# Kernel tuning notes

Hardware: AMD Instinct MI355X
Metric: run time of the kernel (lower is better)

Reference implementation:

```python
import jax, jax.numpy as jnp
import numpy as np

# Acoustic FDTD constants (seistorch-style geometry)
NSHOTS, NT = 4, 512
NZ, NX = 256, 256
NRECS = 128
DT = 1e-3   # s
DH = 10.0   # m grid spacing


def setup_inputs() -> dict:
    key = jax.random.key(0)
    k1, k2, k3, k4, k5, k6 = jax.random.split(key, 6)
    x = jax.random.normal(k1, (NSHOTS, NT), dtype=jnp.float32)  # source wavelets
    # velocity model in [1500, 4000] m/s (CFL: dt*vmax/dh = 0.4 < stability limit)
    vp = 1500.0 + 2500.0 * jax.random.uniform(k2, (NZ, NX), dtype=jnp.float32)
    src_z = jax.random.randint(k3, (NSHOTS,), 0, NZ)
    src_x = jax.random.randint(k4, (NSHOTS,), 0, NX)
    rec_z = jax.random.randint(k5, (NSHOTS, NRECS), 0, NZ)
    rec_x = jax.random.randint(k6, (NSHOTS, NRECS), 0, NX)
    return {"x": x, "vp": vp, "src_z": src_z, "src_x": src_x,
            "rec_z": rec_z, "rec_x": rec_x}


def _laplacian(p):
    # 5-point stencil, zero Dirichlet boundary. p: (B, NZ, NX)
    pp = jnp.pad(p, ((0, 0), (1, 1), (1, 1)))
    return (pp[:, 2:, 1:-1] + pp[:, :-2, 1:-1]
            + pp[:, 1:-1, 2:] + pp[:, 1:-1, :-2]
            - 4.0 * p) / (DH * DH)


def reference(x, vp, src_z, src_x, rec_z, rec_x):
    shots = jnp.arange(NSHOTS)
    c2dt2 = (vp * DT) ** 2  # (NZ, NX), broadcast over shots

    def step(carry, wav_t):
        p_prev, p = carry
        # 2nd-order acoustic update (the PDE "cell")
        p_next = 2.0 * p - p_prev + c2dt2 * _laplacian(p)
        # source scatter-inject (super_source)
        p_next = p_next.at[shots, src_z, src_x].add(wav_t * DT * DT)
        # receiver gather (super_probes): (NSHOTS, NRECS)
        rec = p_next[shots[:, None], rec_z, rec_x]
        return (p, p_next), rec

    p0 = jnp.zeros((NSHOTS, NZ, NX), dtype=x.dtype)
    _, recs = jax.lax.scan(step, (p0, p0), x.T)  # recs: (NT, NSHOTS, NRECS)
    # (shots, time, receivers, n_receiver_types=1)
    return jnp.transpose(recs, (1, 0, 2))[..., None]
```

## Files before the change

### kernel.cpp

```cpp
#include <hip/hip_runtime.h>

#define NSHOTS 4
#define NT     512
#define NZ     256
#define NX     256
#define NRECS  128

static constexpr float DTf    = 0.001f;
static constexpr float INVDH2 = 1.0f / (10.0f * 10.0f);

#define KSTEPS 16
#define TILE   32
#define RPT    8
#define NPAIRS 4
#define NWAVES 8
#define BLOCK  512
#define NWG    (NSHOTS * 64)
#define NPHASE (NT / KSTEPS)
#define LSTRIDE 32

typedef float v2f __attribute__((ext_vector_type(2)));

__device__ __forceinline__ float nbr_left(float v) {
  return __int_as_float(__builtin_amdgcn_update_dpp(
      0, __float_as_int(v), 0x138 , 0xf, 0xf, true));
}
__device__ __forceinline__ float nbr_right(float v) {
  return __int_as_float(__builtin_amdgcn_update_dpp(
      0, __float_as_int(v), 0x130 , 0xf, 0xf, true));
}

__device__ __forceinline__ float gload(const float* p) {
  return __hip_atomic_load(p, __ATOMIC_RELAXED, __HIP_MEMORY_SCOPE_AGENT);
}
__device__ __forceinline__ void gstore(float* p, float v) {
  __hip_atomic_store(p, v, __ATOMIC_RELAXED, __HIP_MEMORY_SCOPE_AGENT);
}
__device__ __forceinline__ unsigned fload(const unsigned* p) {
  return __hip_atomic_load(p, __ATOMIC_RELAXED, __HIP_MEMORY_SCOPE_AGENT);
}
__device__ __forceinline__ void fstore(unsigned* p, unsigned v) {
  __hip_atomic_store(p, v, __ATOMIC_RELAXED, __HIP_MEMORY_SCOPE_AGENT);
}

__global__ __launch_bounds__(BLOCK, 4) void wave_pk(
    float* __restrict__ f0c, float* __restrict__ f0p,
    float* __restrict__ f1c, float* __restrict__ f1p,
    const float* __restrict__ vp, const float* __restrict__ xwav,
    const int* __restrict__ src_z, const int* __restrict__ src_x,
    const int* __restrict__ rec_z, const int* __restrict__ rec_x,
    float* __restrict__ out,
    unsigned* __restrict__ bar)
{
  const int bid  = blockIdx.x;
  const int s    = bid >> 6;
  const int tz   = (bid >> 3) & 7;
  const int tx   = bid & 7;
  const int tid  = threadIdx.x;
  const int w    = tid >> 6;
  const int lane = tid & 63;

  const int gz0 = tz * TILE - KSTEPS;
  const int gx0 = tx * TILE - KSTEPS;
  const int gx  = gx0 + lane;
  const int zb  = w * RPT;

  __shared__ float haloTop[2][NWAVES][64];
  __shared__ float haloBot[2][NWAVES][64];
  __shared__ float recTile[2][TILE][TILE + 1];
  __shared__ int   cntS;
  __shared__ int   lzA[NRECS], lxA[NRECS];
  __shared__ unsigned pkA[NRECS];

  if (tid == 0) cntS = 0;
  __syncthreads();
  if (tid < NRECS) {
    const int lz = rec_z[s * NRECS + tid] - tz * TILE;
    const int lx = rec_x[s * NRECS + tid] - tx * TILE;
    lzA[tid] = lz; lxA[tid] = lx;
    if ((unsigned)lz < (unsigned)TILE && (unsigned)lx < (unsigned)TILE) {
      const int k = atomicAdd(&cntS, 1);
      pkA[k] = (unsigned)tid | ((unsigned)lz << 8) | ((unsigned)lx << 16);
    }
  }
  __syncthreads();
  const int nRec = cntS;
  int myR = 0, myLz = 0, myLx = 0;
  if (tid < nRec) {
    const unsigned p = pkA[tid];
    myR = p & 255; myLz = (p >> 8) & 31; myLx = (p >> 16) & 31;
  }
  const bool wbRow = (w >= 2 && w < 6) && (lane >= KSTEPS && lane < KSTEPS + TILE);
  const int  ilz   = (w - 2) * RPT;
  const int  ilx   = lane - KSTEPS;
  unsigned recMask = 0;
  if (wbRow) {
    for (int r = 0; r < NRECS; ++r)
      if (lxA[r] == ilx && (unsigned)(lzA[r] - ilz) < (unsigned)RPT)
        recMask |= 1u << (lzA[r] - ilz);
  }

  int nb = -1;
  if (tid < 8) {
    const int k  = (tid < 4) ? tid : tid + 1;
    const int dz = k / 3 - 1, dx = k % 3 - 1;
    const int qz = tz + dz, qx = tx + dx;
    if ((unsigned)qz < 8u && (unsigned)qx < 8u)
      nb = (s << 6) | (qz << 3) | qx;
  }
  unsigned* wF = bar;
  unsigned* rF = bar + (size_t)NWG * LSTRIDE;

  auto pollGE = [&](unsigned* base, unsigned target) {
    if (nb >= 0) {
      while (fload(base + (size_t)nb * LSTRIDE) < target)
        __builtin_amdgcn_s_sleep(1);
    }
  };

  const int slz = src_z[s] - gz0;
  const int slx = src_x[s] - gx0;
  const bool srcMine = (slx == lane) && ((unsigned)(slz - zb) < (unsigned)RPT);
  const int  srcI = slz - zb;
  v2f srcM2[NPAIRS];
  #pragma unroll
  for (int p = 0; p < NPAIRS; ++p) {
    srcM2[p].x = (srcMine && srcI == 2 * p)     ? 1.0f : 0.0f;
    srcM2[p].y = (srcMine && srcI == 2 * p + 1) ? 1.0f : 0.0f;
  }

  const bool xok = (unsigned)gx < (unsigned)NX;
  int   offRow[RPT];
  bool  okRow[RPT];
  v2f a2[NPAIRS], b2[NPAIRS], c22[NPAIRS], d22[NPAIRS];
  #pragma unroll
  for (int p = 0; p < NPAIRS; ++p) {
    #pragma unroll
    for (int h = 0; h < 2; ++h) {
      const int i  = 2 * p + h;
      const int gz = gz0 + zb + i;
      const bool ok = xok && ((unsigned)gz < (unsigned)NZ);
      okRow[i]  = ok;
      offRow[i] = ok ? ((s * NZ + gz) * NX + gx) : 0;
      float v = ok ? vp[gz * NX + gx] : 0.0f;
      v *= DTf;
      const float c2 = v * v * INVDH2;
      if (h == 0) { c22[p].x = c2; d22[p].x = 2.0f - 4.0f * c2; }
      else        { c22[p].y = c2; d22[p].y = 2.0f - 4.0f * c2; }
    }
    a2[p] = (v2f)(0.0f); b2[p] = (v2f)(0.0f);
  }

  #pragma unroll 1
  for (int ph = 0; ph < NPHASE; ++ph) {
    const int t0 = ph * KSTEPS;

    if (ph > 0) {
      pollGE(wF, (unsigned)ph);
      __syncthreads();
      const float* rc = (ph & 1) ? f0c : f1c;
      const float* rp = (ph & 1) ? f0p : f1p;
      if (!wbRow) {
        #pragma unroll
        for (int p = 0; p < NPAIRS; ++p) {
          a2[p].x = okRow[2 * p]     ? gload(rc + offRow[2 * p])     : 0.0f;
          a2[p].y = okRow[2 * p + 1] ? gload(rc + offRow[2 * p + 1]) : 0.0f;
          b2[p].x = okRow[2 * p]     ? gload(rp + offRow[2 * p])     : 0.0f;
          b2[p].y = okRow[2 * p + 1] ? gload(rp + offRow[2 * p + 1]) : 0.0f;
        }
      }
      __builtin_amdgcn_s_waitcnt(0);
      __syncthreads();
      if (tid == 0) fstore(rF + (size_t)bid * LSTRIDE, (unsigned)ph);
    }

    float amp[KSTEPS];
    {
      const float4* xw4 = (const float4*)(xwav + s * NT + t0);
      #pragma unroll
      for (int q = 0; q < KSTEPS / 4; ++q) {
        const float4 v = xw4[q];
        amp[4 * q + 0] = (v.x * DTf) * DTf;
        amp[4 * q + 1] = (v.y * DTf) * DTf;
        amp[4 * q + 2] = (v.z * DTf) * DTf;
        amp[4 * q + 3] = (v.w * DTf) * DTf;
      }
    }

    float recv[KSTEPS];

    auto do_step = [&](v2f (&cur)[NPAIRS], v2f (&nxt)[NPAIRS], int tau) {
      const int pb = tau & 1;
      haloTop[pb][w][lane] = cur[0].x;
      haloBot[pb][w][lane] = cur[NPAIRS - 1].y;
      __syncthreads();
      if (tau > 0 && tid < nRec) recv[tau - 1] = recTile[1 - pb][myLz][myLx];
      const float up0 = (w > 0)          ? haloBot[pb][w - 1][lane] : 0.0f;
      const float dn7 = (w < NWAVES - 1) ? haloTop[pb][w + 1][lane] : 0.0f;
      const v2f av = { amp[tau], amp[tau] };
      #pragma unroll
      for (int p = 0; p < NPAIRS; ++p) {
        const float cx = cur[p].x, cy = cur[p].y;
        const float upx = (p == 0)          ? up0 : cur[p - 1].y;
        const float dny = (p == NPAIRS - 1) ? dn7 : cur[p + 1].x;
        v2f ud, lr;
        ud.x = upx + cy;
        ud.y = cx + dny;
        lr.x = nbr_left(cx) + nbr_right(cx);
        lr.y = nbr_left(cy) + nbr_right(cy);
        const v2f sum = ud + lr;
        v2f t = __builtin_elementwise_fma(c22[p], sum, -nxt[p]);
        t = __builtin_elementwise_fma(d22[p], cur[p], t);
        t = __builtin_elementwise_fma(srcM2[p], av, t);
        nxt[p] = t;
      }
      if (recMask) {
        #pragma unroll
        for (int i = 0; i < RPT; ++i)
          if (recMask & (1u << i))
            recTile[pb][ilz + i][ilx] = (i & 1) ? nxt[i >> 1].y : nxt[i >> 1].x;
      }
    };

    #pragma unroll
    for (int h = 0; h < KSTEPS / 2; ++h) {
      do_step(a2, b2, 2 * h);
      do_step(b2, a2, 2 * h + 1);
    }

    if (ph >= 2 && ph != NPHASE - 1) pollGE(rF, (unsigned)(ph - 1));
    __syncthreads();
    if (tid < nRec) recv[KSTEPS - 1] = recTile[1][myLz][myLx];

    if (tid < nRec) {
      #pragma unroll
      for (int t = 0; t < KSTEPS; ++t)
        out[(s * NT + (t0 + t)) * NRECS + myR] = recv[t];
    }

    if (ph != NPHASE - 1) {
      float* wc = (ph & 1) ? f1c : f0c;
      float* wp = (ph & 1) ? f1p : f0p;
      if (wbRow) {
        #pragma unroll
        for (int p = 0; p < NPAIRS; ++p) {
          gstore(wc + offRow[2 * p],     a2[p].x);
          gstore(wc + offRow[2 * p + 1], a2[p].y);
          gstore(wp + offRow[2 * p],     b2[p].x);
          gstore(wp + offRow[2 * p + 1], b2[p].y);
        }
      }
      __builtin_amdgcn_s_waitcnt(0);
      __syncthreads();
      if (tid == 0) fstore(wF + (size_t)bid * LSTRIDE, (unsigned)(ph + 1));
    }
  }
}

extern "C" void kernel_launch(void* const* d_in, const int* in_sizes, int n_in,
                              void* d_out, int out_size, void* d_ws, size_t ws_size,
                              hipStream_t stream) {
  const float* x     = (const float*)d_in[0];
  const float* vp    = (const float*)d_in[1];
  const int*   src_z = (const int*)d_in[2];
  const int*   src_x = (const int*)d_in[3];
  const int*   rec_z = (const int*)d_in[4];
  const int*   rec_x = (const int*)d_in[5];
  float* out = (float*)d_out;

  float* ws = (float*)d_ws;
  const size_t F = (size_t)NSHOTS * NZ * NX;
  float* f0c = ws;
  float* f0p = ws + F;
  float* f1c = ws + 2 * F;
  float* f1p = ws + 3 * F;
  unsigned* bar = (unsigned*)(ws + 4 * F);

  hipMemsetAsync(bar, 0, 2 * (size_t)NWG * LSTRIDE * sizeof(unsigned), stream);

  wave_pk<<<dim3(NWG), dim3(BLOCK), 0, stream>>>(
      f0c, f0p, f1c, f1p, vp, x, src_z, src_x, rec_z, rec_x, out, bar);
}
```

Measured before the change: 324.4 us.

## Triple-buffer halo slabs to drop read-flag barrier and specialize source injection

Replaces the double-buffered exchange fields with three rotating slabs. The separate read-done flags, and the polling on them before overwriting a buffer, can then be removed, leaving only one write-flag wait per phase. Neighbor polling moves from the first threads to lane<8 of every wave, so each wave waits on its own and the block-wide sync after polling is gone. The source FMA is compiled out for tiles whose extended region lacks the source, and the receiver output stores move after the flag publish so they no longer delay neighbors. The cost is more workspace memory and reliance on the three-slab rotation being enough to stop a block overwriting data a slow neighbor has not read yet.

Result: slower. 400.9 us (+23.6%).

```diff
diff --git a/kernel.cpp b/kernel.cpp
--- a/kernel.cpp
+++ b/kernel.cpp
@@ -1,4 +1,5 @@
 #include <hip/hip_runtime.h>
+#include <type_traits>
 
 #define NSHOTS 4
 #define NT     512
@@ -11,13 +12,16 @@
 
 #define KSTEPS 16
 #define TILE   32
+#define EXT    64
 #define RPT    8
 #define NPAIRS 4
 #define NWAVES 8
 #define BLOCK  512
 #define NWG    (NSHOTS * 64)
 #define NPHASE (NT / KSTEPS)
+#define NSLAB  3
 #define LSTRIDE 32
+#define FCNT   (NSHOTS * NZ * NX)
 
 typedef float v2f __attribute__((ext_vector_type(2)));
 
@@ -43,14 +47,13 @@
   __hip_atomic_store(p, v, __ATOMIC_RELAXED, __HIP_MEMORY_SCOPE_AGENT);
 }
 
-__global__ __launch_bounds__(BLOCK, 4) void wave_pk(
-    float* __restrict__ f0c, float* __restrict__ f0p,
-    float* __restrict__ f1c, float* __restrict__ f1p,
+__global__ __launch_bounds__(BLOCK, 4) void wave_pk3(
+    float* __restrict__ fld,
     const float* __restrict__ vp, const float* __restrict__ xwav,
     const int* __restrict__ src_z, const int* __restrict__ src_x,
     const int* __restrict__ rec_z, const int* __restrict__ rec_x,
     float* __restrict__ out,
-    unsigned* __restrict__ bar)
+    unsigned* __restrict__ wF)
 {
   const int bid  = blockIdx.x;
   const int s    = bid >> 6;
@@ -101,25 +104,23 @@
   }
 
   int nb = -1;
-  if (tid < 8) {
-    const int k  = (tid < 4) ? tid : tid + 1;
+  if (lane < 8) {
+    const int k  = (lane < 4) ? lane : lane + 1;
     const int dz = k / 3 - 1, dx = k % 3 - 1;
     const int qz = tz + dz, qx = tx + dx;
     if ((unsigned)qz < 8u && (unsigned)qx < 8u)
       nb = (s << 6) | (qz << 3) | qx;
   }
-  unsigned* wF = bar;
-  unsigned* rF = bar + (size_t)NWG * LSTRIDE;
-
-  auto pollGE = [&](unsigned* base, unsigned target) {
+  auto pollGE = [&](unsigned target) {
     if (nb >= 0) {
-      while (fload(base + (size_t)nb * LSTRIDE) < target)
+      while (fload(wF + (size_t)nb * LSTRIDE) < target)
         __builtin_amdgcn_s_sleep(1);
     }
   };
 
   const int slz = src_z[s] - gz0;
   const int slx = src_x[s] - gx0;
+  const bool srcInExt = ((unsigned)slz < (unsigned)EXT) && ((unsigned)slx < (unsigned)EXT);
   const bool srcMine = (slx == lane) && ((unsigned)(slz - zb) < (unsigned)RPT);
   const int  srcI = slz - zb;
   v2f srcM2[NPAIRS];
@@ -151,15 +152,17 @@
     a2[p] = (v2f)(0.0f); b2[p] = (v2f)(0.0f);
   }
 
+  int wsl = 0;
+
   #pragma unroll 1
   for (int ph = 0; ph < NPHASE; ++ph) {
     const int t0 = ph * KSTEPS;
 
     if (ph > 0) {
-      pollGE(wF, (unsigned)ph);
-      __syncthreads();
-      const float* rc = (ph & 1) ? f0c : f1c;
-      const float* rp = (ph & 1) ? f0p : f1p;
+      pollGE((unsigned)ph);
+      const int rsl = (wsl == 0) ? 2 : wsl - 1;
+      const float* rc = fld + (size_t)(2 * rsl) * FCNT;
+      const float* rp = rc + FCNT;
       if (!wbRow) {
         #pragma unroll
         for (int p = 0; p < NPAIRS; ++p) {
@@ -169,9 +172,6 @@
           b2[p].y = okRow[2 * p + 1] ? gload(rp + offRow[2 * p + 1]) : 0.0f;
         }
       }
-      __builtin_amdgcn_s_waitcnt(0);
-      __syncthreads();
-      if (tid == 0) fstore(rF + (size_t)bid * LSTRIDE, (unsigned)ph);
     }
 
     float amp[KSTEPS];
@@ -189,58 +189,55 @@
 
     float recv[KSTEPS];
 
-    auto do_step = [&](v2f (&cur)[NPAIRS], v2f (&nxt)[NPAIRS], int tau) {
-      const int pb = tau & 1;
-      haloTop[pb][w][lane] = cur[0].x;
-      haloBot[pb][w][lane] = cur[NPAIRS - 1].y;
-      __syncthreads();
-      if (tau > 0 && tid < nRec) recv[tau - 1] = recTile[1 - pb][myLz][myLx];
-      const float up0 = (w > 0)          ? haloBot[pb][w - 1][lane] : 0.0f;
-      const float dn7 = (w < NWAVES - 1) ? haloTop[pb][w + 1][lane] : 0.0f;
-      const v2f av = { amp[tau], amp[tau] };
+    auto run_steps = [&](auto srcc) {
+      auto do_step = [&](v2f (&cur)[NPAIRS], v2f (&nxt)[NPAIRS], int tau) {
+        const int pb = tau & 1;
+        haloTop[pb][w][lane] = cur[0].x;
+        haloBot[pb][w][lane] = cur[NPAIRS - 1].y;
+        __syncthreads();
+        if (tau > 0 && tid < nRec) recv[tau - 1] = recTile[1 - pb][myLz][myLx];
+        const float up0 = (w > 0)          ? haloBot[pb][w - 1][lane] : 0.0f;
+        const float dn7 = (w < NWAVES - 1) ? haloTop[pb][w + 1][lane] : 0.0f;
+        const v2f av = { amp[tau], amp[tau] };
+        #pragma unroll
+        for (int p = 0; p < NPAIRS; ++p) {
+          const float cx = cur[p].x, cy = cur[p].y;
+          const float upx = (p == 0)          ? up0 : cur[p - 1].y;
+          const float dny = (p == NPAIRS - 1) ? dn7 : cur[p + 1].x;
+          v2f ud, lr;
+          ud.x = upx + cy;
+          ud.y = cx + dny;
+          lr.x = nbr_left(cx) + nbr_right(cx);
+          lr.y = nbr_left(cy) + nbr_right(cy);
+          const v2f sum = ud + lr;
+          v2f t = __builtin_elementwise_fma(c22[p], sum, -nxt[p]);
+          t = __builtin_elementwise_fma(d22[p], cur[p], t);
+          if constexpr (decltype(srcc)::value)
+            t = __builtin_elementwise_fma(srcM2[p], av, t);
+          nxt[p] = t;
+        }
+        if (recMask) {
+          #pragma unroll
+          for (int i = 0; i < RPT; ++i)
+            if (recMask & (1u << i))
+              recTile[pb][ilz + i][ilx] = (i & 1) ? nxt[i >> 1].y : nxt[i >> 1].x;
+        }
+      };
       #pragma unroll
-      for (int p = 0; p < NPAIRS; ++p) {
-        const float cx = cur[p].x, cy = cur[p].y;
-        const float upx = (p == 0)          ? up0 : cur[p - 1].y;
-        const float dny = (p == NPAIRS - 1) ? dn7 : cur[p + 1].x;
-        v2f ud, lr;
-        ud.x = upx + cy;
-        ud.y = cx + dny;
-        lr.x = nbr_left(cx) + nbr_right(cx);
-        lr.y = nbr_left(cy) + nbr_right(cy);
-        const v2f sum = ud + lr;
-        v2f t = __builtin_elementwise_fma(c22[p], sum, -nxt[p]);
-        t = __builtin_elementwise_fma(d22[p], cur[p], t);
-        t = __builtin_elementwise_fma(srcM2[p], av, t);
-        nxt[p] = t;
-      }
-      if (recMask) {
-        #pragma unroll
-        for (int i = 0; i < RPT; ++i)
-          if (recMask & (1u << i))
-            recTile[pb][ilz + i][ilx] = (i & 1) ? nxt[i >> 1].y : nxt[i >> 1].x;
+      for (int h = 0; h < KSTEPS / 2; ++h) {
+        do_step(a2, b2, 2 * h);
+        do_step(b2, a2, 2 * h + 1);
       }
     };
-
-    #pragma unroll
-    for (int h = 0; h < KSTEPS / 2; ++h) {
-      do_step(a2, b2, 2 * h);
-      do_step(b2, a2, 2 * h + 1);
-    }
-
-    if (ph >= 2 && ph != NPHASE - 1) pollGE(rF, (unsigned)(ph - 1));
+    if (srcInExt) run_steps(std::true_type{});
+    else          run_steps(std::false_type{});
+
     __syncthreads();
     if (tid < nRec) recv[KSTEPS - 1] = recTile[1][myLz][myLx];
 
-    if (tid < nRec) {
-      #pragma unroll
-      for (int t = 0; t < KSTEPS; ++t)
-        out[(s * NT + (t0 + t)) * NRECS + myR] = recv[t];
-    }
-
     if (ph != NPHASE - 1) {
-      float* wc = (ph & 1) ? f1c : f0c;
-      float* wp = (ph & 1) ? f1p : f0p;
+      float* wc = fld + (size_t)(2 * wsl) * FCNT;
+      float* wp = wc + FCNT;
       if (wbRow) {
         #pragma unroll
         for (int p = 0; p < NPAIRS; ++p) {
@@ -253,6 +250,13 @@
       __builtin_amdgcn_s_waitcnt(0);
       __syncthreads();
       if (tid == 0) fstore(wF + (size_t)bid * LSTRIDE, (unsigned)(ph + 1));
+      wsl = (wsl == 2) ? 0 : wsl + 1;
+    }
+
+    if (tid < nRec) {
+      #pragma unroll
+      for (int t = 0; t < KSTEPS; ++t)
+        out[(s * NT + (t0 + t)) * NRECS + myR] = recv[t];
     }
   }
 }
@@ -268,16 +272,11 @@
   const int*   rec_x = (const int*)d_in[5];
   float* out = (float*)d_out;
 
-  float* ws = (float*)d_ws;
-  const size_t F = (size_t)NSHOTS * NZ * NX;
-  float* f0c = ws;
-  float* f0p = ws + F;
-  float* f1c = ws + 2 * F;
-  float* f1p = ws + 3 * F;
-  unsigned* bar = (unsigned*)(ws + 4 * F);
-
-  hipMemsetAsync(bar, 0, 2 * (size_t)NWG * LSTRIDE * sizeof(unsigned), stream);
-
-  wave_pk<<<dim3(NWG), dim3(BLOCK), 0, stream>>>(
-      f0c, f0p, f1c, f1p, vp, x, src_z, src_x, rec_z, rec_x, out, bar);
-}
+  float* fld = (float*)d_ws;
+  unsigned* wF = (unsigned*)(fld + (size_t)NSLAB * 2 * FCNT);
+
+  hipMemsetAsync(wF, 0, (size_t)NWG * LSTRIDE * sizeof(unsigned), stream);
+
+  wave_pk3<<<dim3(NWG), dim3(BLOCK), 0, stream>>>(
+      fld, vp, x, src_z, src_x, rec_z, rec_x, out, wF);
+}
```

## Drop read-completion flags, specialize source injection, and publish halo flags before output stores

Applied to the files above, without the earlier changes.

Removes the second set of inter-workgroup flags (read-done) and its polling. The write-done flag of phase ph already implies that neighbors finished reading the double buffer being overwritten, so the extra waitcnt, syncthreads and poll per phase can go. It also compiles two versions of the 16-step loop, so tiles whose extended region holds no source skip the source FMA. Finally, the receiver output stores move after the flag publish, so neighbors are released sooner. The cost is more code from duplicated unrolled loops, and correctness now rests on that implicit ordering argument.

Result: slower. 382.4 us (+17.9%).

```diff
diff --git a/kernel.cpp b/kernel.cpp
--- a/kernel.cpp
+++ b/kernel.cpp
@@ -1,4 +1,5 @@
 #include <hip/hip_runtime.h>
+#include <type_traits>
 
 #define NSHOTS 4
 #define NT     512
@@ -11,6 +12,7 @@
 
 #define KSTEPS 16
 #define TILE   32
+#define EXT    64
 #define RPT    8
 #define NPAIRS 4
 #define NWAVES 8
@@ -43,14 +45,14 @@
   __hip_atomic_store(p, v, __ATOMIC_RELAXED, __HIP_MEMORY_SCOPE_AGENT);
 }
 
-__global__ __launch_bounds__(BLOCK, 4) void wave_pk(
+__global__ __launch_bounds__(BLOCK, 4) void wave_pk2(
     float* __restrict__ f0c, float* __restrict__ f0p,
     float* __restrict__ f1c, float* __restrict__ f1p,
     const float* __restrict__ vp, const float* __restrict__ xwav,
     const int* __restrict__ src_z, const int* __restrict__ src_x,
     const int* __restrict__ rec_z, const int* __restrict__ rec_x,
     float* __restrict__ out,
-    unsigned* __restrict__ bar)
+    unsigned* __restrict__ wF)
 {
   const int bid  = blockIdx.x;
   const int s    = bid >> 6;
@@ -108,18 +110,16 @@
     if ((unsigned)qz < 8u && (unsigned)qx < 8u)
       nb = (s << 6) | (qz << 3) | qx;
   }
-  unsigned* wF = bar;
-  unsigned* rF = bar + (size_t)NWG * LSTRIDE;
-
-  auto pollGE = [&](unsigned* base, unsigned target) {
+  auto pollGE = [&](unsigned target) {
     if (nb >= 0) {
-      while (fload(base + (size_t)nb * LSTRIDE) < target)
+      while (fload(wF + (size_t)nb * LSTRIDE) < target)
         __builtin_amdgcn_s_sleep(1);
     }
   };
 
   const int slz = src_z[s] - gz0;
   const int slx = src_x[s] - gx0;
+  const bool srcInExt = ((unsigned)slz < (unsigned)EXT) && ((unsigned)slx < (unsigned)EXT);
   const bool srcMine = (slx == lane) && ((unsigned)(slz - zb) < (unsigned)RPT);
   const int  srcI = slz - zb;
   v2f srcM2[NPAIRS];
@@ -156,7 +156,7 @@
     const int t0 = ph * KSTEPS;
 
     if (ph > 0) {
-      pollGE(wF, (unsigned)ph);
+      pollGE((unsigned)ph);
       __syncthreads();
       const float* rc = (ph & 1) ? f0c : f1c;
       const float* rp = (ph & 1) ? f0p : f1p;
@@ -169,9 +169,6 @@
           b2[p].y = okRow[2 * p + 1] ? gload(rp + offRow[2 * p + 1]) : 0.0f;
         }
       }
-      __builtin_amdgcn_s_waitcnt(0);
-      __syncthreads();
-      if (tid == 0) fstore(rF + (size_t)bid * LSTRIDE, (unsigned)ph);
     }
 
     float amp[KSTEPS];
@@ -189,54 +186,51 @@
 
     float recv[KSTEPS];
 
-    auto do_step = [&](v2f (&cur)[NPAIRS], v2f (&nxt)[NPAIRS], int tau) {
-      const int pb = tau & 1;
-      haloTop[pb][w][lane] = cur[0].x;
-      haloBot[pb][w][lane] = cur[NPAIRS - 1].y;
-      __syncthreads();
-      if (tau > 0 && tid < nRec) recv[tau - 1] = recTile[1 - pb][myLz][myLx];
-      const float up0 = (w > 0)          ? haloBot[pb][w - 1][lane] : 0.0f;
-      const float dn7 = (w < NWAVES - 1) ? haloTop[pb][w + 1][lane] : 0.0f;
-      const v2f av = { amp[tau], amp[tau] };
+    auto run_steps = [&](auto srcc) {
+      auto do_step = [&](v2f (&cur)[NPAIRS], v2f (&nxt)[NPAIRS], int tau) {
+        const int pb = tau & 1;
+        haloTop[pb][w][lane] = cur[0].x;
+        haloBot[pb][w][lane] = cur[NPAIRS - 1].y;
+        __syncthreads();
+        if (tau > 0 && tid < nRec) recv[tau - 1] = recTile[1 - pb][myLz][myLx];
+        const float up0 = (w > 0)          ? haloBot[pb][w - 1][lane] : 0.0f;
+        const float dn7 = (w < NWAVES - 1) ? haloTop[pb][w + 1][lane] : 0.0f;
+        const v2f av = { amp[tau], amp[tau] };
+        #pragma unroll
+        for (int p = 0; p < NPAIRS; ++p) {
+          const float cx = cur[p].x, cy = cur[p].y;
+          const float upx = (p == 0)          ? up0 : cur[p - 1].y;
+          const float dny = (p == NPAIRS - 1) ? dn7 : cur[p + 1].x;
+          v2f ud, lr;
+          ud.x = upx + cy;
+          ud.y = cx + dny;
+          lr.x = nbr_left(cx) + nbr_right(cx);
+          lr.y = nbr_left(cy) + nbr_right(cy);
+          const v2f sum = ud + lr;
+          v2f t = __builtin_elementwise_fma(c22[p], sum, -nxt[p]);
+          t = __builtin_elementwise_fma(d22[p], cur[p], t);
+          if constexpr (decltype(srcc)::value)
+            t = __builtin_elementwise_fma(srcM2[p], av, t);
+          nxt[p] = t;
+        }
+        if (recMask) {
+          #pragma unroll
+          for (int i = 0; i < RPT; ++i)
+            if (recMask & (1u << i))
+              recTile[pb][ilz + i][ilx] = (i & 1) ? nxt[i >> 1].y : nxt[i >> 1].x;
+        }
+      };
       #pragma unroll
-      for (int p = 0; p < NPAIRS; ++p) {
-        const float cx = cur[p].x, cy = cur[p].y;
-        const float upx = (p == 0)          ? up0 : cur[p - 1].y;
-        const float dny = (p == NPAIRS - 1) ? dn7 : cur[p + 1].x;
-        v2f ud, lr;
-        ud.x = upx + cy;
-        ud.y = cx + dny;
-        lr.x = nbr_left(cx) + nbr_right(cx);
-        lr.y = nbr_left(cy) + nbr_right(cy);
-        const v2f sum = ud + lr;
-        v2f t = __builtin_elementwise_fma(c22[p], sum, -nxt[p]);
-        t = __builtin_elementwise_fma(d22[p], cur[p], t);
-        t = __builtin_elementwise_fma(srcM2[p], av, t);
-        nxt[p] = t;
-      }
-      if (recMask) {
-        #pragma unroll
-        for (int i = 0; i < RPT; ++i)
-          if (recMask & (1u << i))
-            recTile[pb][ilz + i][ilx] = (i & 1) ? nxt[i >> 1].y : nxt[i >> 1].x;
+      for (int h = 0; h < KSTEPS / 2; ++h) {
+        do_step(a2, b2, 2 * h);
+        do_step(b2, a2, 2 * h + 1);
       }
     };
-
-    #pragma unroll
-    for (int h = 0; h < KSTEPS / 2; ++h) {
-      do_step(a2, b2, 2 * h);
-      do_step(b2, a2, 2 * h + 1);
-    }
-
-    if (ph >= 2 && ph != NPHASE - 1) pollGE(rF, (unsigned)(ph - 1));
+    if (srcInExt) run_steps(std::true_type{});
+    else          run_steps(std::false_type{});
+
     __syncthreads();
     if (tid < nRec) recv[KSTEPS - 1] = recTile[1][myLz][myLx];
-
-    if (tid < nRec) {
-      #pragma unroll
-      for (int t = 0; t < KSTEPS; ++t)
-        out[(s * NT + (t0 + t)) * NRECS + myR] = recv[t];
-    }
 
     if (ph != NPHASE - 1) {
       float* wc = (ph & 1) ? f1c : f0c;
@@ -254,6 +248,12 @@
       __syncthreads();
       if (tid == 0) fstore(wF + (size_t)bid * LSTRIDE, (unsigned)(ph + 1));
     }
+
+    if (tid < nRec) {
+      #pragma unroll
+      for (int t = 0; t < KSTEPS; ++t)
+        out[(s * NT + (t0 + t)) * NRECS + myR] = recv[t];
+    }
   }
 }
 
@@ -274,10 +274,10 @@
   float* f0p = ws + F;
   float* f1c = ws + 2 * F;
   float* f1p = ws + 3 * F;
-  unsigned* bar = (unsigned*)(ws + 4 * F);
-
-  hipMemsetAsync(bar, 0, 2 * (size_t)NWG * LSTRIDE * sizeof(unsigned), stream);
-
-  wave_pk<<<dim3(NWG), dim3(BLOCK), 0, stream>>>(
-      f0c, f0p, f1c, f1p, vp, x, src_z, src_x, rec_z, rec_x, out, bar);
-}
+  unsigned* wF = (unsigned*)(ws + 4 * F);
+
+  hipMemsetAsync(wF, 0, (size_t)NWG * LSTRIDE * sizeof(unsigned), stream);
+
+  wave_pk2<<<dim3(NWG), dim3(BLOCK), 0, stream>>>(
+      f0c, f0p, f1c, f1p, vp, x, src_z, src_x, rec_z, rec_x, out, wF);
+}
```
